# Kernel tuning notes

Hardware: AMD Instinct MI355X
Metric: run time of the kernel (lower is better)

Reference implementation:

```python
import jax, jax.numpy as jnp
import numpy as np

H, D = 6, 64          # num_heads, head_dim (embed_dim = 384)
WIN = 33              # window_size
PAD = (WIN - 1) // 2  # 16


def setup_inputs() -> dict:
    key = jax.random.key(0)
    ks = jax.random.split(key, 9)
    B, L, E = 8, 1025, 384
    s = 1.0 / np.sqrt(E).astype(np.float32)
    return {
        "x": jax.random.normal(ks[0], (B, L, E), jnp.float32),
        "Wq": jax.random.normal(ks[1], (E, E), jnp.float32) * s,
        "bq": jax.random.normal(ks[2], (E,), jnp.float32) * 0.01,
        "Wk": jax.random.normal(ks[3], (E, E), jnp.float32) * s,
        "bk": jax.random.normal(ks[4], (E,), jnp.float32) * 0.01,
        "Wv": jax.random.normal(ks[5], (E, E), jnp.float32) * s,
        "bv": jax.random.normal(ks[6], (E,), jnp.float32) * 0.01,
        "Wo": jax.random.normal(ks[7], (E, E), jnp.float32) * s,
        "bo": jax.random.normal(ks[8], (E,), jnp.float32) * 0.01,
    }


def reference(x, Wq, bq, Wk, bk, Wv, bv, Wo, bo):
    B, L, E = x.shape
    scale = 1.0 / np.sqrt(D).astype(np.float32)

    def proj(W, b):
        # (B,L,E) -> (B,H,L,D)
        return (x @ W + b).reshape(B, L, H, D).transpose(0, 2, 1, 3)

    Q, K, V = proj(Wq, bq), proj(Wk, bk), proj(Wv, bv)

    # --- cls token (position 0): full attention over all keys ---
    s_cls = jnp.einsum('bhqd,bhkd->bhqk', Q[:, :, :1], K) * scale
    out_cls = jnp.einsum('bhqk,bhkd->bhqd', jax.nn.softmax(s_cls, -1), V)

    # --- remaining tokens: local window + cls appended to every window ---
    Lr = L - 1
    pos = jnp.arange(1, L)                                    # absolute query pos (Lr,)
    idx = pos[:, None] + jnp.arange(WIN)[None, :] - PAD
    # original masks out-of-range AND the cls slot (abs pos 0) inside the window
    valid = (idx >= 1) & (idx < L)
    idxc = jnp.clip(idx, 0, L - 1)

    Kw = K[:, :, idxc]
    Vw = V[:, :, idxc]
    cls_k = jnp.broadcast_to(K[:, :, :1, None, :], (B, H, Lr, 1, D))
    cls_v = jnp.broadcast_to(V[:, :, :1, None, :], (B, H, Lr, 1, D))
    Kw = jnp.concatenate([Kw, cls_k], axis=3)
    Vw = jnp.concatenate([Vw, cls_v], axis=3)
    mask = jnp.concatenate([valid, jnp.ones((Lr, 1), bool)], axis=-1)

    s_rest = jnp.einsum('bhld,bhlwd->bhlw', Q[:, :, 1:], Kw) * scale
    s_rest = jnp.where(mask[None, None], s_rest, -jnp.inf)
    a_rest = jax.nn.softmax(s_rest, axis=-1)
    out_rest = jnp.einsum('bhlw,bhlwd->bhld', a_rest, Vw)

    out = jnp.concatenate([out_cls, out_rest], axis=2)        # (B,H,L,D)
    out = out.transpose(0, 2, 1, 3).reshape(B, L, E)
    return out @ Wo + bo
```

## Files before the change

kernel.cpp:

```cpp
#include <hip/hip_runtime.h>
#include <hip/hip_bf16.h>

typedef unsigned short ushort_t;
typedef __attribute__((ext_vector_type(8))) short short8;
typedef __attribute__((ext_vector_type(4))) float f32x4;

constexpr int Bc = 8;
constexpr int Lc = 1025;
constexpr int Ec = 384;
constexpr int Hc = 6;
constexpr int Dc = 64;
constexpr int MT = Bc * Lc;
constexpr int BHLD = Bc * Hc * Lc * Dc;
constexpr int LT = 1032;
constexpr float SCALE = 0.125f;
constexpr int NCH = 5;

__device__ __forceinline__ float bf2f(ushort_t u) {
    union { unsigned int u; float f; } v; v.u = ((unsigned int)u) << 16; return v.f;
}
__device__ __forceinline__ ushort_t f2bf(float f) {
    union { float f; unsigned int u; } v; v.f = f;
    unsigned int r = v.u + 0x7FFFu + ((v.u >> 16) & 1u);
    return (ushort_t)(r >> 16);
}

#define GLOAD_LDS16(gp, lp)                                                          \
    __builtin_amdgcn_global_load_lds(                                                \
        (const __attribute__((address_space(1))) unsigned int*)(gp),                 \
        (__attribute__((address_space(3))) unsigned int*)(lp), 16, 0, 0)

__global__ __launch_bounds__(256) void prep_kernel(
    const float* __restrict__ x, ushort_t* __restrict__ xb,
    const float* __restrict__ Wq, const float* __restrict__ Wk,
    const float* __restrict__ Wv, const float* __restrict__ Wo,
    ushort_t* __restrict__ Wt_all)
{
    const int bid = blockIdx.x;
    if (bid < 3075) {
        int i = bid * 256 + threadIdx.x;
        float4 v = ((const float4*)x)[i];
        ushort4 o;
        o.x = f2bf(v.x); o.y = f2bf(v.y); o.z = f2bf(v.z); o.w = f2bf(v.w);
        ((ushort4*)xb)[i] = o;
        return;
    }
    __shared__ float t[32][33];
    const int b2 = bid - 3075;
    const int z = b2 / 144, rem = b2 - z * 144;
    const int yy = rem / 12, xx = rem - yy * 12;
    const float* W = (z == 0) ? Wq : (z == 1) ? Wk : (z == 2) ? Wv : Wo;
    ushort_t* Wt = Wt_all + (size_t)z * Ec * Ec;
    const int x0 = xx * 32, y0 = yy * 32;
    const int tx = threadIdx.x & 31, ty = threadIdx.x >> 5;
#pragma unroll
    for (int j = 0; j < 4; j++)
        t[ty + 8 * j][tx] = W[(size_t)(y0 + ty + 8 * j) * Ec + x0 + tx];
    __syncthreads();
#pragma unroll
    for (int j = 0; j < 4; j++)
        Wt[(size_t)(x0 + ty + 8 * j) * Ec + y0 + tx] = f2bf(t[tx][ty + 8 * j]);
}

__global__ __launch_bounds__(256) void qkv_mfma_kernel(
    const ushort_t* __restrict__ xb, const ushort_t* __restrict__ Wt,
    const float* __restrict__ bq, const float* __restrict__ bk,
    const float* __restrict__ bv, ushort_t* __restrict__ qkv)
{
    __shared__ __align__(16) ushort_t As[128 * 64];
    __shared__ __align__(16) ushort_t Bs[128 * 64];

    const int tid = threadIdx.x;
    const int lane = tid & 63;
    const int wid = tid >> 6;
    const int wr = wid >> 1, wc = wid & 1;
    const int m0 = blockIdx.x * 128;
    const int n0 = blockIdx.y * 128;
    const int which = n0 / Ec;
    const int nm0 = n0 - which * Ec;
    const ushort_t* Wmat = Wt + (size_t)which * Ec * Ec;
    const float* bias = (which == 0) ? bq : (which == 1) ? bk : bv;

    f32x4 acc[4][4];
#pragma unroll
    for (int i = 0; i < 4; i++)
#pragma unroll
        for (int j = 0; j < 4; j++) acc[i][j] = (f32x4){0.f, 0.f, 0.f, 0.f};

    for (int kt = 0; kt < Ec; kt += 64) {
#pragma unroll
        for (int c = 0; c < 4; c++) {
            int ci  = (wid * 4 + c) * 64 + lane;
            int row = ci >> 3, kc = ci & 7;
            int kcs = kc ^ (row & 7);
            int rowA = m0 + row; rowA = rowA < MT ? rowA : MT - 1;
            GLOAD_LDS16(xb + (size_t)rowA * Ec + kt + kcs * 8,
                        As + (size_t)(wid * 4 + c) * 512);
            GLOAD_LDS16(Wmat + (size_t)(nm0 + row) * Ec + kt + kcs * 8,
                        Bs + (size_t)(wid * 4 + c) * 512);
        }
        __syncthreads();

#pragma unroll
        for (int ki = 0; ki < 2; ki++) {
            short8 a[4], b[4];
            const int kchunk = ki * 4 + (lane >> 4);
#pragma unroll
            for (int mi = 0; mi < 4; mi++) {
                int row = wr * 64 + mi * 16 + (lane & 15);
                a[mi] = *(const short8*)(As + row * 64 + ((kchunk ^ (row & 7)) * 8));
            }
#pragma unroll
            for (int ni = 0; ni < 4; ni++) {
                int row = wc * 64 + ni * 16 + (lane & 15);
                b[ni] = *(const short8*)(Bs + row * 64 + ((kchunk ^ (row & 7)) * 8));
            }
#pragma unroll
            for (int mi = 0; mi < 4; mi++)
#pragma unroll
                for (int ni = 0; ni < 4; ni++)
                    acc[mi][ni] = __builtin_amdgcn_mfma_f32_16x16x32_bf16(
                        a[mi], b[ni], acc[mi][ni], 0, 0, 0);
        }
        __syncthreads();
    }

    const int colL = lane & 15;
    const int rowL = (lane >> 4) * 4;
#pragma unroll
    for (int ni = 0; ni < 4; ni++) {
        int nm = nm0 + wc * 64 + ni * 16 + colL;
        float bv_ = bias[nm];
        int h = nm >> 6, d = nm & 63;
#pragma unroll
        for (int mi = 0; mi < 4; mi++) {
#pragma unroll
            for (int r = 0; r < 4; r++) {
                int m = m0 + wr * 64 + mi * 16 + rowL + r;
                if (m < MT) {
                    int b_ = m / Lc, l = m - b_ * Lc;
                    qkv[(size_t)which * BHLD +
                        ((size_t)(b_ * Hc + h) * Lc + l) * Dc + d] =
                        f2bf(acc[mi][ni][r] + bv_);
                }
            }
        }
    }
}

__global__ __launch_bounds__(256) void vt_cls_kernel(
    const ushort_t* __restrict__ qkv, ushort_t* __restrict__ vt,
    float* __restrict__ part)
{
    const int bh = blockIdx.y;
    const int tid = threadIdx.x;

    if (blockIdx.x < 17) {
        __shared__ ushort_t t[64][68];
        const int l0 = blockIdx.x * 64;
        const ushort_t* V = qkv + 2 * (size_t)BHLD + (size_t)bh * Lc * Dc;
        ushort_t* vto = vt + (size_t)bh * 64 * LT;
#pragma unroll
        for (int i = 0; i < 4; i++) {
            int idx = tid + i * 256;
            int l = idx >> 4, dc = idx & 15;
            int ls = l0 + l; ls = ls > 1024 ? 1024 : ls;
            ushort4 v = *(const ushort4*)(V + (size_t)ls * Dc + dc * 4);
            *(ushort4*)&t[l][dc * 4] = v;
        }
        __syncthreads();
#pragma unroll
        for (int i = 0; i < 4; i++) {
            int idx = tid + i * 256;
            int d = idx >> 4, lc = idx & 15;
            ushort4 o;
            o.x = t[lc * 4 + 0][d]; o.y = t[lc * 4 + 1][d];
            o.z = t[lc * 4 + 2][d]; o.w = t[lc * 4 + 3][d];
            int lw = l0 + lc * 4;
            if (lw <= 1024)
                *(ushort4*)(vto + (size_t)d * LT + lw) = o;
        }
        return;
    }

    __shared__ float qs[64];
    __shared__ float ps[256];
    __shared__ float red[256];

    const int ch = blockIdx.x - 17;
    const int base = ch * 256;
    const int count = min(256, Lc - base);
    const ushort_t* Q = qkv + (size_t)bh * Lc * Dc;
    const ushort_t* K = Q + (size_t)BHLD;
    const ushort_t* V = Q + 2 * (size_t)BHLD;

    if (tid < 64) qs[tid] = bf2f(Q[tid]);
    __syncthreads();

    float s = -1e30f;
    if (tid < count) {
        const ushort4* kp = (const ushort4*)(K + (size_t)(base + tid) * Dc);
        float acc = 0.f;
#pragma unroll
        for (int c = 0; c < 16; c++) {
            ushort4 kv = kp[c];
            acc += qs[c * 4 + 0] * bf2f(kv.x) + qs[c * 4 + 1] * bf2f(kv.y) +
                   qs[c * 4 + 2] * bf2f(kv.z) + qs[c * 4 + 3] * bf2f(kv.w);
        }
        s = acc * SCALE;
    }
    red[tid] = s; __syncthreads();
    for (int off = 128; off > 0; off >>= 1) {
        if (tid < off) red[tid] = fmaxf(red[tid], red[tid + off]);
        __syncthreads();
    }
    const float m = red[0];
    __syncthreads();

    float p = (tid < count) ? __expf(s - m) : 0.f;
    ps[tid] = p;
    red[tid] = p; __syncthreads();
    for (int off = 128; off > 0; off >>= 1) {
        if (tid < off) red[tid] += red[tid + off];
        __syncthreads();
    }
    const float S = red[0];
    __syncthreads();

    const int d = tid & 63, sl = tid >> 6;
    float acc = 0.f;
    for (int i = sl; i < count; i += 4)
        acc += ps[i] * bf2f(V[(size_t)(base + i) * Dc + d]);
    red[tid] = acc; __syncthreads();
    if (tid < 64) {
        float o = red[tid] + red[tid + 64] + red[tid + 128] + red[tid + 192];
        float* pp = part + (size_t)(bh * NCH + ch) * 66;
        pp[2 + tid] = o;
        if (tid == 0) { pp[0] = m; pp[1] = S; }
    }
}

__global__ __launch_bounds__(256) void win_attn_kernel(
    const ushort_t* __restrict__ qkv, const ushort_t* __restrict__ vt,
    const float* __restrict__ part, ushort_t* __restrict__ attnb)
{
    __shared__ __align__(16) ushort_t Kb[128 * 64];
    __shared__ __align__(16) ushort_t Vb[64 * 128];
    __shared__ __align__(16) ushort_t QP[64 * 128];

    const int bh = blockIdx.y;
    const int tid = threadIdx.x, lane = tid & 63, wid = tid >> 6;
    const int b_ = bh / Hc, h = bh - b_ * Hc;

    if (blockIdx.x == 16) {
        if (tid >= 64) return;
        float M = -1e30f;
#pragma unroll
        for (int ch = 0; ch < NCH; ch++)
            M = fmaxf(M, part[(size_t)(bh * NCH + ch) * 66]);
        float S = 0.f, O = 0.f;
#pragma unroll
        for (int ch = 0; ch < NCH; ch++) {
            const float* pp = part + (size_t)(bh * NCH + ch) * 66;
            float w = __expf(pp[0] - M);
            S += pp[1] * w;
            O += pp[2 + tid] * w;
        }
        attnb[(size_t)(b_ * Lc) * Ec + h * 64 + tid] = f2bf(O / S);
        return;
    }

    const int t = blockIdx.x;
    const int l0 = 1 + t * 64, k0 = l0 - 17;
    const ushort_t* Qg = qkv + (size_t)bh * Lc * Dc;
    const ushort_t* Kg = Qg + (size_t)BHLD;
    const ushort_t* Vt = vt + (size_t)bh * 64 * LT;

#pragma unroll
    for (int i = 0; i < 4; i++) {
        int p = (i * 4 + wid) * 64 + lane;
        {
            int j = p >> 3, c = p & 7, g = c ^ (j & 7);
            int kp = (j <= 111) ? min(max(k0 + j, 0), 1024) : 0;
            GLOAD_LDS16(Kg + (size_t)kp * Dc + g * 8,
                        Kb + (size_t)(i * 4 + wid) * 512);
        }
        {
            int d = p >> 4, jc = p & 15, g = jc ^ (d & 15);
            int kb = (g <= 13) ? max(k0 + g * 8, 0) : 0;
            GLOAD_LDS16(Vt + (size_t)d * LT + kb,
                        Vb + (size_t)(i * 4 + wid) * 512);
        }
    }
#pragma unroll
    for (int i = 0; i < 2; i++) {
        int p = (i * 4 + wid) * 64 + lane;
        int q = p >> 3, c = p & 7, g = c ^ (q & 7);
        GLOAD_LDS16(Qg + (size_t)(l0 + q) * Dc + g * 8,
                    QP + (size_t)(i * 4 + wid) * 512);
    }
    __syncthreads();

    f32x4 sacc[8];
#pragma unroll
    for (int tj = 0; tj < 8; tj++) sacc[tj] = (f32x4){0.f, 0.f, 0.f, 0.f};
#pragma unroll
    for (int ki = 0; ki < 2; ki++) {
        const int gc = ki * 4 + (lane >> 4);
        const int qrow = wid * 16 + (lane & 15);
        short8 a = *(const short8*)(QP + qrow * 64 + ((gc ^ (qrow & 7)) * 8));
#pragma unroll
        for (int tj = 0; tj < 8; tj++) {
            int jrow = tj * 16 + (lane & 15);
            short8 b = *(const short8*)(Kb + jrow * 64 + ((gc ^ (jrow & 7)) * 8));
            sacc[tj] = __builtin_amdgcn_mfma_f32_16x16x32_bf16(a, b, sacc[tj], 0, 0, 0);
        }
    }
    __syncthreads();

    const int qb = wid * 16 + (lane >> 4) * 4;
    const int cl = lane & 15;
    float inv[4];
#pragma unroll
    for (int r = 0; r < 4; r++) {
        const int q = qb + r;
        float sv[8];
        float mx = -1e30f;
#pragma unroll
        for (int tj = 0; tj < 8; tj++) {
            int j = tj * 16 + cl;
            int kp = k0 + j;
            bool valid = (j == 112) ||
                         ((j >= q + 1) && (j <= q + 33) && (kp >= 1) && (kp <= 1024));
            float s = valid ? sacc[tj][r] * SCALE : -1e30f;
            sv[tj] = s;
            mx = fmaxf(mx, s);
        }
        mx = fmaxf(mx, __shfl_xor(mx, 1));
        mx = fmaxf(mx, __shfl_xor(mx, 2));
        mx = fmaxf(mx, __shfl_xor(mx, 4));
        mx = fmaxf(mx, __shfl_xor(mx, 8));
        float sum = 0.f;
#pragma unroll
        for (int tj = 0; tj < 8; tj++) {
            float pv = __expf(sv[tj] - mx);
            sv[tj] = pv;
            sum += pv;
        }
        sum += __shfl_xor(sum, 1);
        sum += __shfl_xor(sum, 2);
        sum += __shfl_xor(sum, 4);
        sum += __shfl_xor(sum, 8);
        inv[r] = 1.f / sum;
#pragma unroll
        for (int tj = 0; tj < 8; tj++) {
            int j = tj * 16 + cl;
            QP[q * 128 + (((j >> 3) ^ (q & 15)) * 8) + (j & 7)] = f2bf(sv[tj]);
        }
    }
    __syncthreads();

    f32x4 oacc[4];
#pragma unroll
    for (int dt = 0; dt < 4; dt++) oacc[dt] = (f32x4){0.f, 0.f, 0.f, 0.f};
#pragma unroll
    for (int kc = 0; kc < 4; kc++) {
        const int gc = kc * 4 + (lane >> 4);
        const int qrow = wid * 16 + (lane & 15);
        short8 pa = *(const short8*)(QP + qrow * 128 + ((gc ^ (qrow & 15)) * 8));
#pragma unroll
        for (int dt = 0; dt < 4; dt++) {
            int drow = dt * 16 + (lane & 15);
            short8 vb = *(const short8*)(Vb + drow * 128 + ((gc ^ (drow & 15)) * 8));
            oacc[dt] = __builtin_amdgcn_mfma_f32_16x16x32_bf16(pa, vb, oacc[dt], 0, 0, 0);
        }
    }

#pragma unroll
    for (int dt = 0; dt < 4; dt++) {
        int d = dt * 16 + cl;
#pragma unroll
        for (int r = 0; r < 4; r++) {
            int l = l0 + qb + r;
            attnb[(size_t)(b_ * Lc + l) * Ec + h * 64 + d] = f2bf(oacc[dt][r] * inv[r]);
        }
    }
}

__global__ __launch_bounds__(256) void out_mfma_kernel(
    const ushort_t* __restrict__ attn_rows, const ushort_t* __restrict__ Wot,
    const float* __restrict__ bo, float* __restrict__ out)
{
    __shared__ __align__(16) ushort_t As[64 * 64];
    __shared__ __align__(16) ushort_t Bs[128 * 64];

    const int tid = threadIdx.x;
    const int lane = tid & 63;
    const int wid = tid >> 6;
    const int wr = wid & 1, wc = wid >> 1;
    const int m0 = blockIdx.x * 64;
    const int n0 = blockIdx.y * 128;

    f32x4 acc[2][4];
#pragma unroll
    for (int i = 0; i < 2; i++)
#pragma unroll
        for (int j = 0; j < 4; j++) acc[i][j] = (f32x4){0.f, 0.f, 0.f, 0.f};

    for (int kt = 0; kt < Ec; kt += 64) {
#pragma unroll
        for (int c = 0; c < 2; c++) {
            int ci  = (wid * 2 + c) * 64 + lane;
            int row = ci >> 3, kc = ci & 7;
            int kcs = kc ^ (row & 7);
            int rowA = m0 + row; rowA = rowA < MT ? rowA : MT - 1;
            GLOAD_LDS16(attn_rows + (size_t)rowA * Ec + kt + kcs * 8,
                        As + (size_t)(wid * 2 + c) * 512);
        }
#pragma unroll
        for (int c = 0; c < 4; c++) {
            int ci  = (wid * 4 + c) * 64 + lane;
            int row = ci >> 3, kc = ci & 7;
            int kcs = kc ^ (row & 7);
            GLOAD_LDS16(Wot + (size_t)(n0 + row) * Ec + kt + kcs * 8,
                        Bs + (size_t)(wid * 4 + c) * 512);
        }
        __syncthreads();

#pragma unroll
        for (int ki = 0; ki < 2; ki++) {
            short8 a[2], b[4];
            const int kchunk = ki * 4 + (lane >> 4);
#pragma unroll
            for (int mi = 0; mi < 2; mi++) {
                int row = wr * 32 + mi * 16 + (lane & 15);
                a[mi] = *(const short8*)(As + row * 64 + ((kchunk ^ (row & 7)) * 8));
            }
#pragma unroll
            for (int ni = 0; ni < 4; ni++) {
                int row = wc * 64 + ni * 16 + (lane & 15);
                b[ni] = *(const short8*)(Bs + row * 64 + ((kchunk ^ (row & 7)) * 8));
            }
#pragma unroll
            for (int mi = 0; mi < 2; mi++)
#pragma unroll
                for (int ni = 0; ni < 4; ni++)
                    acc[mi][ni] = __builtin_amdgcn_mfma_f32_16x16x32_bf16(
                        a[mi], b[ni], acc[mi][ni], 0, 0, 0);
        }
        __syncthreads();
    }

    const int colL = lane & 15;
    const int rowL = (lane >> 4) * 4;
#pragma unroll
    for (int ni = 0; ni < 4; ni++) {
        int n = n0 + wc * 64 + ni * 16 + colL;
        float bo_v = bo[n];
#pragma unroll
        for (int mi = 0; mi < 2; mi++) {
#pragma unroll
            for (int r = 0; r < 4; r++) {
                int m = m0 + wr * 32 + mi * 16 + rowL + r;
                if (m < MT) out[(size_t)m * Ec + n] = acc[mi][ni][r] + bo_v;
            }
        }
    }
}

extern "C" void kernel_launch(void* const* d_in, const int* in_sizes, int n_in,
                              void* d_out, int out_size, void* d_ws, size_t ws_size,
                              hipStream_t stream)
{
    const float* x  = (const float*)d_in[0];
    const float* Wq = (const float*)d_in[1];
    const float* bq = (const float*)d_in[2];
    const float* Wk = (const float*)d_in[3];
    const float* bk = (const float*)d_in[4];
    const float* Wv = (const float*)d_in[5];
    const float* bv = (const float*)d_in[6];
    const float* Wo = (const float*)d_in[7];
    const float* bo = (const float*)d_in[8];
    float* out = (float*)d_out;

    ushort_t* xb    = (ushort_t*)d_ws;
    ushort_t* Wt    = xb + (size_t)MT * Ec;
    ushort_t* qkvb  = Wt + (size_t)4 * Ec * Ec;
    ushort_t* vtb   = qkvb + (size_t)3 * BHLD;
    ushort_t* attnb = vtb + (size_t)Bc * Hc * 64 * LT;
    float* clsp     = (float*)(attnb + (size_t)MT * Ec);

    prep_kernel<<<3075 + 576, 256, 0, stream>>>(x, xb, Wq, Wk, Wv, Wo, Wt);

    qkv_mfma_kernel<<<dim3((MT + 127) / 128, 9), 256, 0, stream>>>(
        xb, Wt, bq, bk, bv, qkvb);

    vt_cls_kernel<<<dim3(17 + NCH, Bc * Hc), 256, 0, stream>>>(qkvb, vtb, clsp);

    win_attn_kernel<<<dim3(17, Bc * Hc), 256, 0, stream>>>(qkvb, vtb, clsp, attnb);

    out_mfma_kernel<<<dim3((MT + 63) / 64, 3), 256, 0, stream>>>(
        attnb, Wt + (size_t)3 * Ec * Ec, bo, out);
}
```

Before: 165.2 us.

## Fuse V transpose into window attention and shrink key window to 96 rows

```diff
diff --git a/kernel.cpp b/kernel.cpp
--- a/kernel.cpp
+++ b/kernel.cpp
@@ -12,7 +12,6 @@
 constexpr int Dc = 64;
 constexpr int MT = Bc * Lc;
 constexpr int BHLD = Bc * Hc * Lc * Dc;
-constexpr int LT = 1032;
 constexpr float SCALE = 0.125f;
 constexpr int NCH = 5;
 
@@ -148,52 +147,21 @@
     }
 }
 
-__global__ __launch_bounds__(256) void vt_cls_kernel(
-    const ushort_t* __restrict__ qkv, ushort_t* __restrict__ vt,
-    float* __restrict__ part)
+__global__ __launch_bounds__(256) void cls_part_kernel(
+    const ushort_t* __restrict__ qkv, float* __restrict__ part)
 {
-    const int bh = blockIdx.y;
-    const int tid = threadIdx.x;
-
-    if (blockIdx.x < 17) {
-        __shared__ ushort_t t[64][68];
-        const int l0 = blockIdx.x * 64;
-        const ushort_t* V = qkv + 2 * (size_t)BHLD + (size_t)bh * Lc * Dc;
-        ushort_t* vto = vt + (size_t)bh * 64 * LT;
-#pragma unroll
-        for (int i = 0; i < 4; i++) {
-            int idx = tid + i * 256;
-            int l = idx >> 4, dc = idx & 15;
-            int ls = l0 + l; ls = ls > 1024 ? 1024 : ls;
-            ushort4 v = *(const ushort4*)(V + (size_t)ls * Dc + dc * 4);
-            *(ushort4*)&t[l][dc * 4] = v;
-        }
-        __syncthreads();
-#pragma unroll
-        for (int i = 0; i < 4; i++) {
-            int idx = tid + i * 256;
-            int d = idx >> 4, lc = idx & 15;
-            ushort4 o;
-            o.x = t[lc * 4 + 0][d]; o.y = t[lc * 4 + 1][d];
-            o.z = t[lc * 4 + 2][d]; o.w = t[lc * 4 + 3][d];
-            int lw = l0 + lc * 4;
-            if (lw <= 1024)
-                *(ushort4*)(vto + (size_t)d * LT + lw) = o;
-        }
-        return;
-    }
-
-    __shared__ float qs[64];
-    __shared__ float ps[256];
-    __shared__ float red[256];
-
-    const int ch = blockIdx.x - 17;
+    const int bh = blockIdx.x, ch = blockIdx.y;
     const int base = ch * 256;
     const int count = min(256, Lc - base);
     const ushort_t* Q = qkv + (size_t)bh * Lc * Dc;
     const ushort_t* K = Q + (size_t)BHLD;
     const ushort_t* V = Q + 2 * (size_t)BHLD;
 
+    __shared__ float qs[64];
+    __shared__ float ps[256];
+    __shared__ float red[256];
+
+    const int tid = threadIdx.x;
     if (tid < 64) qs[tid] = bf2f(Q[tid]);
     __syncthreads();
 
@@ -241,8 +209,8 @@
 }
 
 __global__ __launch_bounds__(256) void win_attn_kernel(
-    const ushort_t* __restrict__ qkv, const ushort_t* __restrict__ vt,
-    const float* __restrict__ part, ushort_t* __restrict__ attnb)
+    const ushort_t* __restrict__ qkv, const float* __restrict__ part,
+    ushort_t* __restrict__ attnb)
 {
     __shared__ __align__(16) ushort_t Kb[128 * 64];
     __shared__ __align__(16) ushort_t Vb[64 * 128];
@@ -271,25 +239,34 @@
     }
 
     const int t = blockIdx.x;
-    const int l0 = 1 + t * 64, k0 = l0 - 17;
+    const int l0 = 1 + t * 64;
+    const int k0n = l0 - 16;
     const ushort_t* Qg = qkv + (size_t)bh * Lc * Dc;
     const ushort_t* Kg = Qg + (size_t)BHLD;
-    const ushort_t* Vt = vt + (size_t)bh * 64 * LT;
-
+    const ushort_t* Vg = Qg + 2 * (size_t)BHLD;
+
+    short8 vreg[4];
+    int vrow[4], vdc[4];
 #pragma unroll
     for (int i = 0; i < 4; i++) {
-        int p = (i * 4 + wid) * 64 + lane;
-        {
+        int ci = i * 256 + tid;
+        if (ci < 896) {
+            int j = ci >> 3, dc = ci & 7;
+            int kp = (j <= 95) ? min(max(k0n + j, 0), 1024) : 0;
+            vreg[i] = *(const short8*)(Vg + (size_t)kp * Dc + dc * 8);
+            vrow[i] = j; vdc[i] = dc;
+        } else { vrow[i] = -1; vdc[i] = 0; }
+    }
+
+#pragma unroll
+    for (int i = 0; i < 4; i++) {
+        int wchunk = i * 4 + wid;
+        if (wchunk < 14) {
+            int p = wchunk * 64 + lane;
             int j = p >> 3, c = p & 7, g = c ^ (j & 7);
-            int kp = (j <= 111) ? min(max(k0 + j, 0), 1024) : 0;
+            int kp = (j <= 95) ? min(max(k0n + j, 0), 1024) : 0;
             GLOAD_LDS16(Kg + (size_t)kp * Dc + g * 8,
-                        Kb + (size_t)(i * 4 + wid) * 512);
-        }
-        {
-            int d = p >> 4, jc = p & 15, g = jc ^ (d & 15);
-            int kb = (g <= 13) ? max(k0 + g * 8, 0) : 0;
-            GLOAD_LDS16(Vt + (size_t)d * LT + kb,
-                        Vb + (size_t)(i * 4 + wid) * 512);
+                        Kb + (size_t)wchunk * 512);
         }
     }
 #pragma unroll
@@ -299,18 +276,35 @@
         GLOAD_LDS16(Qg + (size_t)(l0 + q) * Dc + g * 8,
                     QP + (size_t)(i * 4 + wid) * 512);
     }
-    __syncthreads();
-
-    f32x4 sacc[8];
-#pragma unroll
-    for (int tj = 0; tj < 8; tj++) sacc[tj] = (f32x4){0.f, 0.f, 0.f, 0.f};
+
+#pragma unroll
+    for (int i = 0; i < 4; i++) {
+        if (vrow[i] >= 0) {
+            int j = vrow[i], jc3 = j >> 3, j7 = j & 7;
+#pragma unroll
+            for (int z = 0; z < 8; z++) {
+                int d = vdc[i] * 8 + z;
+                Vb[d * 128 + ((jc3 ^ (d & 15)) * 8) + j7] = (ushort_t)vreg[i][z];
+            }
+        }
+    }
+    if (tid < 128) {
+        int d = tid >> 1, lcn = 14 + (tid & 1);
+        *(short8*)(Vb + d * 128 + ((lcn ^ (d & 15)) * 8)) =
+            (short8){0, 0, 0, 0, 0, 0, 0, 0};
+    }
+    __syncthreads();
+
+    f32x4 sacc[7];
+#pragma unroll
+    for (int tj = 0; tj < 7; tj++) sacc[tj] = (f32x4){0.f, 0.f, 0.f, 0.f};
 #pragma unroll
     for (int ki = 0; ki < 2; ki++) {
         const int gc = ki * 4 + (lane >> 4);
         const int qrow = wid * 16 + (lane & 15);
         short8 a = *(const short8*)(QP + qrow * 64 + ((gc ^ (qrow & 7)) * 8));
 #pragma unroll
-        for (int tj = 0; tj < 8; tj++) {
+        for (int tj = 0; tj < 7; tj++) {
             int jrow = tj * 16 + (lane & 15);
             short8 b = *(const short8*)(Kb + jrow * 64 + ((gc ^ (jrow & 7)) * 8));
             sacc[tj] = __builtin_amdgcn_mfma_f32_16x16x32_bf16(a, b, sacc[tj], 0, 0, 0);
@@ -324,14 +318,14 @@
 #pragma unroll
     for (int r = 0; r < 4; r++) {
         const int q = qb + r;
-        float sv[8];
+        float sv[7];
         float mx = -1e30f;
 #pragma unroll
-        for (int tj = 0; tj < 8; tj++) {
+        for (int tj = 0; tj < 7; tj++) {
             int j = tj * 16 + cl;
-            int kp = k0 + j;
-            bool valid = (j == 112) ||
-                         ((j >= q + 1) && (j <= q + 33) && (kp >= 1) && (kp <= 1024));
+            int kp = k0n + j;
+            bool valid = (j == 96) ||
+                         ((j >= q) && (j <= q + 32) && (kp >= 1) && (kp <= 1024));
             float s = valid ? sacc[tj][r] * SCALE : -1e30f;
             sv[tj] = s;
             mx = fmaxf(mx, s);
@@ -342,7 +336,7 @@
         mx = fmaxf(mx, __shfl_xor(mx, 8));
         float sum = 0.f;
 #pragma unroll
-        for (int tj = 0; tj < 8; tj++) {
+        for (int tj = 0; tj < 7; tj++) {
             float pv = __expf(sv[tj] - mx);
             sv[tj] = pv;
             sum += pv;
@@ -353,9 +347,19 @@
         sum += __shfl_xor(sum, 8);
         inv[r] = 1.f / sum;
 #pragma unroll
-        for (int tj = 0; tj < 8; tj++) {
+        for (int tj = 0; tj < 7; tj++) {
             int j = tj * 16 + cl;
             QP[q * 128 + (((j >> 3) ^ (q & 15)) * 8) + (j & 7)] = f2bf(sv[tj]);
+        }
+    }
+    if (cl == 0) {
+#pragma unroll
+        for (int r = 0; r < 4; r++) {
+            int q = qb + r;
+            *(short8*)(QP + q * 128 + ((14 ^ (q & 15)) * 8)) =
+                (short8){0, 0, 0, 0, 0, 0, 0, 0};
+            *(short8*)(QP + q * 128 + ((15 ^ (q & 15)) * 8)) =
+                (short8){0, 0, 0, 0, 0, 0, 0, 0};
         }
     }
     __syncthreads();
@@ -486,8 +490,7 @@
     ushort_t* xb    = (ushort_t*)d_ws;
     ushort_t* Wt    = xb + (size_t)MT * Ec;
     ushort_t* qkvb  = Wt + (size_t)4 * Ec * Ec;
-    ushort_t* vtb   = qkvb + (size_t)3 * BHLD;
-    ushort_t* attnb = vtb + (size_t)Bc * Hc * 64 * LT;
+    ushort_t* attnb = qkvb + (size_t)3 * BHLD;
     float* clsp     = (float*)(attnb + (size_t)MT * Ec);
 
     prep_kernel<<<3075 + 576, 256, 0, stream>>>(x, xb, Wq, Wk, Wv, Wo, Wt);
@@ -495,9 +498,9 @@
     qkv_mfma_kernel<<<dim3((MT + 127) / 128, 9), 256, 0, stream>>>(
         xb, Wt, bq, bk, bv, qkvb);
 
-    vt_cls_kernel<<<dim3(17 + NCH, Bc * Hc), 256, 0, stream>>>(qkvb, vtb, clsp);
-
-    win_attn_kernel<<<dim3(17, Bc * Hc), 256, 0, stream>>>(qkvb, vtb, clsp, attnb);
+    cls_part_kernel<<<dim3(Bc * Hc, NCH), 256, 0, stream>>>(qkvb, clsp);
+
+    win_attn_kernel<<<dim3(17, Bc * Hc), 256, 0, stream>>>(qkvb, clsp, attnb);
 
     out_mfma_kernel<<<dim3((MT + 63) / 64, 3), 256, 0, stream>>>(
         attnb, Wt + (size_t)3 * Ec * Ec, bo, out);
```

After: 163.9 us. About the same (-0.8%).
